# Performance work log

Hardware: AMD Instinct MI355X
Metric: run time of the kernel (lower is better)

The kernel has to match this reference:

```python
import jax, jax.numpy as jnp
import numpy as np

VOCAB, EMB, H1, H2, T, B = 21, 128, 64, 100, 500, 1024


def lstm(x, W_ih, W_hh, b_ih, b_hh):
    # x: [B, T, D]; torch gate order i, f, g, o
    Bx, H = x.shape[0], W_hh.shape[1]
    xproj = jnp.einsum('btd,gd->btg', x, W_ih) + b_ih  # [B, T, 4H]

    def step(carry, xt):
        h, c = carry
        gates = xt + h @ W_hh.T + b_hh
        i, f, g, o = jnp.split(gates, 4, axis=-1)
        c = jax.nn.sigmoid(f) * c + jax.nn.sigmoid(i) * jnp.tanh(g)
        h = jax.nn.sigmoid(o) * jnp.tanh(c)
        return (h, c), h

    h0 = jnp.zeros((Bx, H), x.dtype)
    _, hs = jax.lax.scan(step, (h0, h0), xproj.transpose(1, 0, 2))
    return hs.transpose(1, 0, 2)  # [B, T, H]


def setup_inputs() -> dict:
    key = jax.random.key(0)
    ks = jax.random.split(key, 12)
    s = 0.05
    x_idx = jax.random.randint(ks[0], (B, T), 0, VOCAB, dtype=jnp.int32)
    emb_table = jax.random.normal(ks[1], (VOCAB, EMB), jnp.float32) * s
    emb_table = emb_table.at[0].set(0.0)  # padding_idx=0
    d = dict(
        x_idx=x_idx,
        emb_table=emb_table,
        W_ih1=jax.random.normal(ks[2], (4 * H1, EMB), jnp.float32) * s,
        W_hh1=jax.random.normal(ks[3], (4 * H1, H1), jnp.float32) * s,
        b_ih1=jax.random.normal(ks[4], (4 * H1,), jnp.float32) * s,
        b_hh1=jax.random.normal(ks[5], (4 * H1,), jnp.float32) * s,
        W_ih2=jax.random.normal(ks[6], (4 * H2, H1), jnp.float32) * s,
        W_hh2=jax.random.normal(ks[7], (4 * H2, H2), jnp.float32) * s,
        b_ih2=jax.random.normal(ks[8], (4 * H2,), jnp.float32) * s,
        b_hh2=jax.random.normal(ks[9], (4 * H2,), jnp.float32) * s,
        fc_w=jax.random.normal(ks[10], (1, H2), jnp.float32) * s,
        fc_b=jax.random.normal(ks[11], (1,), jnp.float32) * s,
    )
    return d


def reference(x_idx, emb_table, W_ih1, W_hh1, b_ih1, b_hh1,
              W_ih2, W_hh2, b_ih2, b_hh2, fc_w, fc_b):
    # embedding with padding_idx=0 (row is zero; mask keeps grads faithful)
    x = emb_table[x_idx] * (x_idx != 0)[..., None].astype(emb_table.dtype)  # [B,T,128]
    x = lstm(x, W_ih1, W_hh1, b_ih1, b_hh1)  # [B,T,64]
    # MaxPool1d(kernel=5, stride=5) over time
    Bx, Tx, D = x.shape
    Tp = Tx // 5
    x = x[:, :Tp * 5].reshape(Bx, Tp, 5, D).max(axis=2)  # [B,T/5,64]
    x = lstm(x, W_ih2, W_hh2, b_ih2, b_hh2)  # [B,T/5,100]
    h = x[:, -1, :]
    return jax.nn.sigmoid(h @ fc_w.T + fc_b)  # [B,1]
```

## Files before the change

### kernel.cpp

```cpp
#include <hip/hip_runtime.h>

#define VOCAB 21
#define EMB 128
#define H1 64
#define H2 100
#define T1 500
#define TP 100
#define NB 1024
#define TBL_LD 260
#define LOG2E 1.44269504f

typedef __attribute__((ext_vector_type(8))) short bf16x8;
typedef __attribute__((ext_vector_type(4))) float f32x4;

__device__ __forceinline__ unsigned short f2bf(float x){
    union { float f; unsigned u; } v; v.f = x;
    return (unsigned short)((v.u + 0x8000u) >> 16);
}
__device__ __forceinline__ void bar_lds(){
    asm volatile("s_waitcnt lgkmcnt(0)\n\ts_barrier" ::: "memory");
}
__device__ __forceinline__ void wait_lds(){
    asm volatile("s_waitcnt lgkmcnt(0)" ::: "memory");
}
__device__ __forceinline__ float ex2(float x){ return __builtin_amdgcn_exp2f(x); }
__device__ __forceinline__ float rcp(float x){ return __builtin_amdgcn_rcpf(x); }

__global__ void k_table(const float* __restrict__ Wih, const float* __restrict__ emb,
                        const float* __restrict__ bih, const float* __restrict__ bhh,
                        float* __restrict__ table){
    const int p = threadIdx.x;
    const int v = blockIdx.x;
    const int orig = (p & 3) * H1 + (p >> 2);
    float s = bih[orig] + bhh[orig];
    if (v != 0){
        const float* w = Wih + orig * EMB;
        const float* e = emb + v * EMB;
        #pragma unroll 16
        for (int d = 0; d < EMB; ++d) s += w[d]*e[d];
    }
    table[v*TBL_LD + p] = s * LOG2E;
}

__global__ __launch_bounds__(1024, 1) void k_lstm1(
    const int* __restrict__ xidx, const float* __restrict__ Whh,
    const float* __restrict__ tbl_g, unsigned short* __restrict__ x2b){
  __shared__ __align__(16) float table[VOCAB*TBL_LD];
  __shared__ __align__(16) unsigned short hbuf[2][16*64];
  __shared__ int idxs[16*T1];

  const int tid = threadIdx.x;
  const int gt = tid >> 6, l = tid & 63;
  const int b0 = blockIdx.x * 16;
  const int row = l & 15, kg = l >> 4;

  for (int i = tid; i < VOCAB*TBL_LD; i += 1024) table[i] = tbl_g[i];
  for (int i = tid; i < 16*T1; i += 1024){
      int r = i / T1, t = i - r*T1;
      idxs[i] = xidx[(b0 + r)*T1 + t];
  }
  { unsigned short* hz = (unsigned short*)hbuf;
    for (int i = tid; i < 2048; i += 1024) hz[i] = 0; }

  bf16x8 af0, af1;
  {
      const int p = 16*gt + row;
      const int orig = (p & 3)*H1 + (p >> 2);
      bf16x8 f;
      const float* s0 = Whh + orig*H1 + kg*8;
      #pragma unroll
      for (int j = 0; j < 8; ++j) f[j] = (short)f2bf(s0[j] * LOG2E);
      af0 = f;
      const float* s1 = Whh + orig*H1 + 32 + kg*8;
      #pragma unroll
      for (int j = 0; j < 8; ++j) f[j] = (short)f2bf(s1[j] * LOG2E);
      af1 = f;
  }

  char* hb = (char*)hbuf;
  const int swz = (row & 7) << 4;
  const int rb0 = (row*128 + 16*kg) ^ swz;
  const int rb1 = (row*128 + 64 + 16*kg) ^ swz;
  const int cell = 4*gt + kg;
  const int wbh  = (row*128 + 2*cell) ^ swz;
  const float twoL = 2.0f * LOG2E;

  float cc = 0.f, pm = -1e30f;
  __syncthreads();

  int vv = idxs[row*T1];
  f32x4 tq = *(const f32x4*)&table[vv*TBL_LD + 4*cell];
  int vnext = idxs[row*T1 + 1];

  int rp = 0, tm = 0, tp = 0;
  for (int t = 0; t < T1; ++t){
      bf16x8 bf0 = *(const bf16x8*)(hb + rp + rb0);
      bf16x8 bf1 = *(const bf16x8*)(hb + rp + rb1);
      f32x4 a = __builtin_amdgcn_mfma_f32_16x16x32_bf16(af0, bf0, tq, 0,0,0);
      f32x4 z = __builtin_amdgcn_mfma_f32_16x16x32_bf16(af1, bf1, a, 0,0,0);
      f32x4 tqn = *(const f32x4*)&table[vnext*TBL_LD + 4*cell];
      int vn2 = idxs[row*T1 + ((t + 2 < T1) ? (t + 2) : 0)];
      float si = rcp(1.f + ex2(-z[0]));
      float sf = rcp(1.f + ex2(-z[1]));
      float so = rcp(1.f + ex2(-z[3]));
      float tg = 1.f - 2.f*rcp(1.f + ex2(z[2] + z[2]));
      cc = sf*cc + si*tg;
      float th = 1.f - 2.f*rcp(1.f + ex2(twoL*cc));
      float h = so*th;
      const int wp = rp ^ 2048;
      *(unsigned short*)(hb + wp + wbh) = f2bf(h);
      pm = fmaxf(pm, h);
      if (++tm == 5){
          x2b[(b0 + row)*(TP*H1) + tp*H1 + cell] = f2bf(pm);
          pm = -1e30f; tm = 0; ++tp;
      }
      tq = tqn; vnext = vn2;
      rp = wp;
      bar_lds();
  }
}

__global__ __launch_bounds__(512, 1) void k_lstm2(
    const unsigned short* __restrict__ x2b, const float* __restrict__ Wih,
    const float* __restrict__ Whh, const float* __restrict__ bih,
    const float* __restrict__ bhh, const float* __restrict__ fcw,
    const float* __restrict__ fcb, float* __restrict__ out){
  __shared__ __align__(16) unsigned short blds[2][16*128];
  __shared__ __align__(16) f32x4 gl2[108*4];
  __shared__ float fcred[8][4];

  const int tid = threadIdx.x;
  const int w = tid >> 6, l = tid & 63;
  const int b0 = blockIdx.x * 4;
  const int n = l & 15, kg = l >> 4;
  const int tlo = (w < 2) ? 4*w : 8 + 3*(w - 2);
  const int nt  = (w < 2) ? 4 : 3;

  { unsigned short* bz0 = (unsigned short*)blds;
    for (int i = tid; i < 4096; i += 512) bz0[i] = 0; }
  { float* gz = (float*)gl2;
    for (int i = tid; i < 432*4; i += 512) gz[i] = 0.f; }

  bf16x8 af[4][6];
  #pragma unroll
  for (int u = 0; u < 4; ++u){
      if (u < nt){
          const int p = 16*(tlo + u) + n;
          const int cell_ = p >> 2, gate = p & 3;
          #pragma unroll
          for (int c = 0; c < 6; ++c){
              bf16x8 f;
              #pragma unroll
              for (int jj = 0; jj < 8; ++jj){
                  int k = c*32 + kg*8 + jj;
                  float vv = 0.f;
                  if (cell_ < H2){
                      if (k < 64)           vv = Wih[(gate*H2 + cell_)*H1 + k];
                      else if (k < 64 + H2) vv = Whh[(gate*H2 + cell_)*H2 + (k - 64)];
                  }
                  f[jj] = (short)f2bf(vv * LOG2E);
              }
              af[u][c] = f;
          }
      }
  }

  f32x4 bz[4];
  #pragma unroll
  for (int u = 0; u < 4; ++u){
      const int cu = 4*(tlo + u) + kg;
      f32x4 b = {0.f,0.f,0.f,0.f};
      if (u < nt && cu < H2){
          #pragma unroll
          for (int g = 0; g < 4; ++g) b[g] = (bih[g*H2 + cu] + bhh[g*H2 + cu]) * LOG2E;
      }
      bz[u] = b;
  }

  const bool act = (l >> 2) < 4*nt;
  const int cellc = 4*tlo + (l >> 2);
  const int r_c = l & 3;
  const float fwv = (act && cellc < H2) ? fcw[cellc] : 0.f;
  const float twoL = 2.0f * LOG2E;

  char* bb = (char*)blds;
  char* gb = (char*)gl2;
  int rbh[4];
  #pragma unroll
  for (int j = 0; j < 4; ++j)
      rbh[j] = (n*256 + 2*(j*32 + 8*kg)) ^ ((n & 7) << 4);
  const int wbh = (r_c*256 + 2*cellc) ^ ((r_c & 7) << 4);

  const int nr = n & 3;
  const unsigned short* xrow = x2b + (b0 + nr)*(TP*H1) + kg*8;
  bf16x8 x0 = *(const bf16x8*)(xrow);
  bf16x8 x1 = *(const bf16x8*)(xrow + 32);
  float cc = 0.f, hv = 0.f;
  __syncthreads();

  int rp = 0;
  for (int t = 0; t < TP; ++t){
      bf16x8 xn0, xn1;
      if (t + 1 < TP){
          xn0 = *(const bf16x8*)(xrow + (t+1)*H1);
          xn1 = *(const bf16x8*)(xrow + (t+1)*H1 + 32);
      }
      bf16x8 h0 = *(const bf16x8*)(bb + rp + rbh[0]);
      bf16x8 h1 = *(const bf16x8*)(bb + rp + rbh[1]);
      bf16x8 h2 = *(const bf16x8*)(bb + rp + rbh[2]);
      bf16x8 h3 = *(const bf16x8*)(bb + rp + rbh[3]);
      #pragma unroll
      for (int u = 0; u < 4; ++u){
          if (u < nt){
              f32x4 za = __builtin_amdgcn_mfma_f32_16x16x32_bf16(af[u][0], x0, bz[u], 0,0,0);
              f32x4 zb = __builtin_amdgcn_mfma_f32_16x16x32_bf16(af[u][1], x1, (f32x4){0.f,0.f,0.f,0.f}, 0,0,0);
              za = __builtin_amdgcn_mfma_f32_16x16x32_bf16(af[u][2], h0, za, 0,0,0);
              zb = __builtin_amdgcn_mfma_f32_16x16x32_bf16(af[u][3], h1, zb, 0,0,0);
              za = __builtin_amdgcn_mfma_f32_16x16x32_bf16(af[u][4], h2, za, 0,0,0);
              zb = __builtin_amdgcn_mfma_f32_16x16x32_bf16(af[u][5], h3, zb, 0,0,0);
              f32x4 z = za + zb;
              if (n < 4)
                  *(f32x4*)(gb + 256*(tlo + u) + 64*kg + 16*n) = z;
          }
      }
      wait_lds();
      const int wp = rp ^ 4096;
      if (act){
          f32x4 q = *(const f32x4*)(gb + 256*tlo + 16*l);
          float si = rcp(1.f + ex2(-q[0]));
          float sf = rcp(1.f + ex2(-q[1]));
          float so = rcp(1.f + ex2(-q[3]));
          float tg = 1.f - 2.f*rcp(1.f + ex2(q[2] + q[2]));
          cc = sf*cc + si*tg;
          float th = 1.f - 2.f*rcp(1.f + ex2(twoL*cc));
          hv = so*th;
          *(unsigned short*)(bb + wp + wbh) = f2bf(hv);
      }
      x0 = xn0; x1 = xn1;
      rp = wp;
      bar_lds();
  }

  float p = (act && cellc < H2) ? hv * fwv : 0.f;
  p += __shfl_xor(p, 4);
  p += __shfl_xor(p, 8);
  p += __shfl_xor(p, 16);
  p += __shfl_xor(p, 32);
  if (l < 4) fcred[w][l] = p;
  __syncthreads();
  if (tid < 4){
      float s = 0.f;
      #pragma unroll
      for (int ww = 0; ww < 8; ++ww) s += fcred[ww][tid];
      s += fcb[0];
      out[b0 + tid] = rcp(1.f + ex2(-s * LOG2E));
  }
}

extern "C" void kernel_launch(void* const* d_in, const int* in_sizes, int n_in,
                              void* d_out, int out_size, void* d_ws, size_t ws_size,
                              hipStream_t stream) {
    const int*   x_idx = (const int*)  d_in[0];
    const float* emb   = (const float*)d_in[1];
    const float* Wih1  = (const float*)d_in[2];
    const float* Whh1  = (const float*)d_in[3];
    const float* bih1  = (const float*)d_in[4];
    const float* bhh1  = (const float*)d_in[5];
    const float* Wih2  = (const float*)d_in[6];
    const float* Whh2  = (const float*)d_in[7];
    const float* bih2  = (const float*)d_in[8];
    const float* bhh2  = (const float*)d_in[9];
    const float* fcw   = (const float*)d_in[10];
    const float* fcb   = (const float*)d_in[11];
    float* out = (float*)d_out;

    float*          table = (float*)d_ws;
    unsigned short* x2b   = (unsigned short*)((char*)d_ws + 32768);

    k_table<<<VOCAB, 256, 0, stream>>>(Wih1, emb, bih1, bhh1, table);
    k_lstm1<<<NB / 16, 1024, 0, stream>>>(x_idx, Whh1, table, x2b);
    k_lstm2<<<NB / 4, 512, 0, stream>>>(x2b, Wih2, Whh2, bih2, bhh2, fcw, fcb, out);
}
```

Before: 305.7 us.

## Split LSTM1 into 8-row batches per block with LDS gate redistribution

Layer-1 now processes 8 sequences per 512-thread block instead of 16 per 1024-thread block, doubling the grid to 128 blocks. Each wave issues two MFMA tiles, of which only 8 of the 16 columns are useful. It then stages the results through LDS so that every lane gets a full gate quad for one cell and row. The intent is to spread the latency-bound recurrence over more CUs and shorten the per-step barrier group. The cost is an extra LDS write, a wait and a read on every time step, plus wasted MFMA columns. The hbuf zero loop still clears 2048 entries although the buffer is now half that size, which relies on the adjacent LDS being overwritten later.

```diff
diff --git a/kernel.cpp b/kernel.cpp
--- a/kernel.cpp
+++ b/kernel.cpp
@@ -42,47 +42,53 @@
     table[v*TBL_LD + p] = s * LOG2E;
 }
 
-__global__ __launch_bounds__(1024, 1) void k_lstm1(
+__global__ __launch_bounds__(512, 1) void k_lstm1(
     const int* __restrict__ xidx, const float* __restrict__ Whh,
     const float* __restrict__ tbl_g, unsigned short* __restrict__ x2b){
   __shared__ __align__(16) float table[VOCAB*TBL_LD];
-  __shared__ __align__(16) unsigned short hbuf[2][16*64];
-  __shared__ int idxs[16*T1];
+  __shared__ __align__(16) unsigned short hbuf[2][8*64];
+  __shared__ __align__(16) f32x4 glds[8][64];
+  __shared__ int idxs[8*T1];
 
   const int tid = threadIdx.x;
-  const int gt = tid >> 6, l = tid & 63;
-  const int b0 = blockIdx.x * 16;
-  const int row = l & 15, kg = l >> 4;
-
-  for (int i = tid; i < VOCAB*TBL_LD; i += 1024) table[i] = tbl_g[i];
-  for (int i = tid; i < 16*T1; i += 1024){
+  const int w = tid >> 6, l = tid & 63;
+  const int b0 = blockIdx.x * 8;
+  const int n = l & 15, kg = l >> 4;
+
+  for (int i = tid; i < VOCAB*TBL_LD; i += 512) table[i] = tbl_g[i];
+  for (int i = tid; i < 8*T1; i += 512){
       int r = i / T1, t = i - r*T1;
       idxs[i] = xidx[(b0 + r)*T1 + t];
   }
   { unsigned short* hz = (unsigned short*)hbuf;
-    for (int i = tid; i < 2048; i += 1024) hz[i] = 0; }
-
-  bf16x8 af0, af1;
-  {
-      const int p = 16*gt + row;
+    for (int i = tid; i < 2048; i += 512) hz[i] = 0; }
+
+  bf16x8 af[2][2];
+  #pragma unroll
+  for (int u = 0; u < 2; ++u){
+      const int p = 16*(2*w + u) + n;
       const int orig = (p & 3)*H1 + (p >> 2);
-      bf16x8 f;
-      const float* s0 = Whh + orig*H1 + kg*8;
       #pragma unroll
-      for (int j = 0; j < 8; ++j) f[j] = (short)f2bf(s0[j] * LOG2E);
-      af0 = f;
-      const float* s1 = Whh + orig*H1 + 32 + kg*8;
-      #pragma unroll
-      for (int j = 0; j < 8; ++j) f[j] = (short)f2bf(s1[j] * LOG2E);
-      af1 = f;
+      for (int c = 0; c < 2; ++c){
+          const float* src = Whh + orig*H1 + c*32 + kg*8;
+          bf16x8 f;
+          #pragma unroll
+          for (int j = 0; j < 8; ++j) f[j] = (short)f2bf(src[j] * LOG2E);
+          af[u][c] = f;
+      }
   }
 
   char* hb = (char*)hbuf;
-  const int swz = (row & 7) << 4;
-  const int rb0 = (row*128 + 16*kg) ^ swz;
-  const int rb1 = (row*128 + 64 + 16*kg) ^ swz;
-  const int cell = 4*gt + kg;
-  const int wbh  = (row*128 + 2*cell) ^ swz;
+  char* gb = (char*)glds + 1024*w;
+  const int rbr = n & 7;
+  const int swzB = rbr << 4;
+  const int rb0 = (rbr*128 + 16*kg) ^ swzB;
+  const int rb1 = (rbr*128 + 64 + 16*kg) ^ swzB;
+  const int gw0 = 128*kg + 16*(n & 7);
+  const int gw1 = 512 + gw0;
+  const int cell = 8*w + 4*(l >> 5) + ((l >> 3) & 3);
+  const int row  = l & 7;
+  const int wbh  = (row*128 + 2*cell) ^ (row << 4);
   const float twoL = 2.0f * LOG2E;
 
   float cc = 0.f, pm = -1e30f;
@@ -91,23 +97,36 @@
   int vv = idxs[row*T1];
   f32x4 tq = *(const f32x4*)&table[vv*TBL_LD + 4*cell];
   int vnext = idxs[row*T1 + 1];
+  const f32x4 z4 = {0.f, 0.f, 0.f, 0.f};
 
   int rp = 0, tm = 0, tp = 0;
   for (int t = 0; t < T1; ++t){
       bf16x8 bf0 = *(const bf16x8*)(hb + rp + rb0);
       bf16x8 bf1 = *(const bf16x8*)(hb + rp + rb1);
-      f32x4 a = __builtin_amdgcn_mfma_f32_16x16x32_bf16(af0, bf0, tq, 0,0,0);
-      f32x4 z = __builtin_amdgcn_mfma_f32_16x16x32_bf16(af1, bf1, a, 0,0,0);
+      f32x4 a0 = __builtin_amdgcn_mfma_f32_16x16x32_bf16(af[0][0], bf0, z4, 0,0,0);
+      a0       = __builtin_amdgcn_mfma_f32_16x16x32_bf16(af[0][1], bf1, a0, 0,0,0);
+      f32x4 a1 = __builtin_amdgcn_mfma_f32_16x16x32_bf16(af[1][0], bf0, z4, 0,0,0);
+      a1       = __builtin_amdgcn_mfma_f32_16x16x32_bf16(af[1][1], bf1, a1, 0,0,0);
+      if (n < 8){
+          *(f32x4*)(gb + gw0) = a0;
+          *(f32x4*)(gb + gw1) = a1;
+      }
+      wait_lds();
+      f32x4 q = *(const f32x4*)(gb + 16*l);
       f32x4 tqn = *(const f32x4*)&table[vnext*TBL_LD + 4*cell];
       int vn2 = idxs[row*T1 + ((t + 2 < T1) ? (t + 2) : 0)];
-      float si = rcp(1.f + ex2(-z[0]));
-      float sf = rcp(1.f + ex2(-z[1]));
-      float so = rcp(1.f + ex2(-z[3]));
-      float tg = 1.f - 2.f*rcp(1.f + ex2(z[2] + z[2]));
+      float gi = q[0] + tq[0];
+      float gf = q[1] + tq[1];
+      float gg = q[2] + tq[2];
+      float go = q[3] + tq[3];
+      float si = rcp(1.f + ex2(-gi));
+      float sf = rcp(1.f + ex2(-gf));
+      float so = rcp(1.f + ex2(-go));
+      float tg = 1.f - 2.f*rcp(1.f + ex2(gg + gg));
       cc = sf*cc + si*tg;
       float th = 1.f - 2.f*rcp(1.f + ex2(twoL*cc));
       float h = so*th;
-      const int wp = rp ^ 2048;
+      const int wp = rp ^ 1024;
       *(unsigned short*)(hb + wp + wbh) = f2bf(h);
       pm = fmaxf(pm, h);
       if (++tm == 5){
@@ -278,6 +297,6 @@
     unsigned short* x2b   = (unsigned short*)((char*)d_ws + 32768);
 
     k_table<<<VOCAB, 256, 0, stream>>>(Wih1, emb, bih1, bhh1, table);
-    k_lstm1<<<NB / 16, 1024, 0, stream>>>(x_idx, Whh1, table, x2b);
+    k_lstm1<<<NB / 8, 512, 0, stream>>>(x_idx, Whh1, table, x2b);
     k_lstm2<<<NB / 4, 512, 0, stream>>>(x2b, Wih2, Whh2, bih2, bhh2, fcw, fcb, out);
 }
```

New measurement: 328.4 us. 1.07x slower.

## Process 16 sequences per LSTM2 block and apply gates in MFMA registers

Applied to the files above, without the earlier changes.

The second LSTM kernel now fills all 16 MFMA columns with distinct batch rows (16 sequences per block instead of 4), cutting its grid from 256 to 64 blocks. Gate nonlinearities are computed directly on the MFMA accumulator registers, so the per-step LDS staging buffer and its extra wait are gone. Each lane now keeps four cell states, so it does more transcendental work per step, and the lower block count may leave many CUs idle on the serial recurrence.

```diff
diff --git a/kernel.cpp b/kernel.cpp
--- a/kernel.cpp
+++ b/kernel.cpp
@@ -19,9 +19,6 @@
 }
 __device__ __forceinline__ void bar_lds(){
     asm volatile("s_waitcnt lgkmcnt(0)\n\ts_barrier" ::: "memory");
-}
-__device__ __forceinline__ void wait_lds(){
-    asm volatile("s_waitcnt lgkmcnt(0)" ::: "memory");
 }
 __device__ __forceinline__ float ex2(float x){ return __builtin_amdgcn_exp2f(x); }
 __device__ __forceinline__ float rcp(float x){ return __builtin_amdgcn_rcpf(x); }
@@ -126,20 +123,17 @@
     const float* __restrict__ bhh, const float* __restrict__ fcw,
     const float* __restrict__ fcb, float* __restrict__ out){
   __shared__ __align__(16) unsigned short blds[2][16*128];
-  __shared__ __align__(16) f32x4 gl2[108*4];
-  __shared__ float fcred[8][4];
+  __shared__ float fcred[8][16];
 
   const int tid = threadIdx.x;
   const int w = tid >> 6, l = tid & 63;
-  const int b0 = blockIdx.x * 4;
+  const int b0 = blockIdx.x * 16;
   const int n = l & 15, kg = l >> 4;
   const int tlo = (w < 2) ? 4*w : 8 + 3*(w - 2);
   const int nt  = (w < 2) ? 4 : 3;
 
   { unsigned short* bz0 = (unsigned short*)blds;
     for (int i = tid; i < 4096; i += 512) bz0[i] = 0; }
-  { float* gz = (float*)gl2;
-    for (int i = tid; i < 432*4; i += 512) gz[i] = 0.f; }
 
   bf16x8 af[4][6];
   #pragma unroll
@@ -166,36 +160,34 @@
   }
 
   f32x4 bz[4];
+  int cu[4], wbh[4];
+  float fw[4];
   #pragma unroll
   for (int u = 0; u < 4; ++u){
-      const int cu = 4*(tlo + u) + kg;
+      cu[u] = 4*(tlo + u) + kg;
       f32x4 b = {0.f,0.f,0.f,0.f};
-      if (u < nt && cu < H2){
+      float fv = 0.f;
+      if (u < nt && cu[u] < H2){
           #pragma unroll
-          for (int g = 0; g < 4; ++g) b[g] = (bih[g*H2 + cu] + bhh[g*H2 + cu]) * LOG2E;
-      }
-      bz[u] = b;
-  }
-
-  const bool act = (l >> 2) < 4*nt;
-  const int cellc = 4*tlo + (l >> 2);
-  const int r_c = l & 3;
-  const float fwv = (act && cellc < H2) ? fcw[cellc] : 0.f;
+          for (int g = 0; g < 4; ++g) b[g] = (bih[g*H2 + cu[u]] + bhh[g*H2 + cu[u]]) * LOG2E;
+          fv = fcw[cu[u]];
+      }
+      bz[u] = b; fw[u] = fv;
+      wbh[u] = (n*256 + 2*cu[u]) ^ ((n & 7) << 4);
+  }
   const float twoL = 2.0f * LOG2E;
 
   char* bb = (char*)blds;
-  char* gb = (char*)gl2;
   int rbh[4];
   #pragma unroll
   for (int j = 0; j < 4; ++j)
       rbh[j] = (n*256 + 2*(j*32 + 8*kg)) ^ ((n & 7) << 4);
-  const int wbh = (r_c*256 + 2*cellc) ^ ((r_c & 7) << 4);
-
-  const int nr = n & 3;
-  const unsigned short* xrow = x2b + (b0 + nr)*(TP*H1) + kg*8;
+
+  const unsigned short* xrow = x2b + (b0 + n)*(TP*H1) + kg*8;
   bf16x8 x0 = *(const bf16x8*)(xrow);
   bf16x8 x1 = *(const bf16x8*)(xrow + 32);
-  float cc = 0.f, hv = 0.f;
+  float cc[4] = {0.f,0.f,0.f,0.f};
+  float hv[4] = {0.f,0.f,0.f,0.f};
   __syncthreads();
 
   int rp = 0;
@@ -209,6 +201,7 @@
       bf16x8 h1 = *(const bf16x8*)(bb + rp + rbh[1]);
       bf16x8 h2 = *(const bf16x8*)(bb + rp + rbh[2]);
       bf16x8 h3 = *(const bf16x8*)(bb + rp + rbh[3]);
+      const int wp = rp ^ 4096;
       #pragma unroll
       for (int u = 0; u < 4; ++u){
           if (u < nt){
@@ -219,36 +212,31 @@
               za = __builtin_amdgcn_mfma_f32_16x16x32_bf16(af[u][4], h2, za, 0,0,0);
               zb = __builtin_amdgcn_mfma_f32_16x16x32_bf16(af[u][5], h3, zb, 0,0,0);
               f32x4 z = za + zb;
-              if (n < 4)
-                  *(f32x4*)(gb + 256*(tlo + u) + 64*kg + 16*n) = z;
+              float si = rcp(1.f + ex2(-z[0]));
+              float sf = rcp(1.f + ex2(-z[1]));
+              float so = rcp(1.f + ex2(-z[3]));
+              float tg = 1.f - 2.f*rcp(1.f + ex2(z[2] + z[2]));
+              cc[u] = sf*cc[u] + si*tg;
+              float th = 1.f - 2.f*rcp(1.f + ex2(twoL*cc[u]));
+              hv[u] = so*th;
+              if (cu[u] < H2)
+                  *(unsigned short*)(bb + wp + wbh[u]) = f2bf(hv[u]);
           }
-      }
-      wait_lds();
-      const int wp = rp ^ 4096;
-      if (act){
-          f32x4 q = *(const f32x4*)(gb + 256*tlo + 16*l);
-          float si = rcp(1.f + ex2(-q[0]));
-          float sf = rcp(1.f + ex2(-q[1]));
-          float so = rcp(1.f + ex2(-q[3]));
-          float tg = 1.f - 2.f*rcp(1.f + ex2(q[2] + q[2]));
-          cc = sf*cc + si*tg;
-          float th = 1.f - 2.f*rcp(1.f + ex2(twoL*cc));
-          hv = so*th;
-          *(unsigned short*)(bb + wp + wbh) = f2bf(hv);
       }
       x0 = xn0; x1 = xn1;
       rp = wp;
       bar_lds();
   }
 
-  float p = (act && cellc < H2) ? hv * fwv : 0.f;
-  p += __shfl_xor(p, 4);
-  p += __shfl_xor(p, 8);
+  float p = 0.f;
+  #pragma unroll
+  for (int u = 0; u < 4; ++u)
+      if (u < nt && cu[u] < H2) p += hv[u] * fw[u];
   p += __shfl_xor(p, 16);
   p += __shfl_xor(p, 32);
-  if (l < 4) fcred[w][l] = p;
+  if (l < 16) fcred[w][l] = p;
   __syncthreads();
-  if (tid < 4){
+  if (tid < 16){
       float s = 0.f;
       #pragma unroll
       for (int ww = 0; ww < 8; ++ww) s += fcred[ww][tid];
@@ -279,5 +267,5 @@
 
     k_table<<<VOCAB, 256, 0, stream>>>(Wih1, emb, bih1, bhh1, table);
     k_lstm1<<<NB / 16, 1024, 0, stream>>>(x_idx, Whh1, table, x2b);
-    k_lstm2<<<NB / 4, 512, 0, stream>>>(x2b, Wih2, Whh2, bih2, bhh2, fcw, fcb, out);
-}
+    k_lstm2<<<NB / 16, 512, 0, stream>>>(x2b, Wih2, Whh2, bih2, bhh2, fcw, fcb, out);
+}
```

Measured after the change: 312.3 us. +2.1%, slower.
